# Optimization experiments

Measured on AMD Instinct MI355X. Metric: run time of the kernel, lower is better.

## Reference

```python
import jax, jax.numpy as jnp
import numpy as np

B, T, C = 4, 4096, 256
H = 4
D = C // H
EPS = 1e-5


def layer_norm(x, w, b):
    mean = x.mean(axis=-1, keepdims=True)
    var = x.var(axis=-1, keepdims=True)
    return w * (x - mean) / jnp.sqrt(var + EPS) + b


def setup_inputs() -> dict:
    key = jax.random.key(0)
    ks = jax.random.split(key, 8)
    s = lambda n: 1.0 / np.sqrt(n)
    return {
        "x": jax.random.normal(ks[0], (B, T, C), jnp.float32),
        "qkv_w": jax.random.normal(ks[1], (C, 3 * C), jnp.float32) * s(C),
        "qkv_b": jnp.zeros((3 * C,), jnp.float32),
        "proj_w": jax.random.normal(ks[2], (C, C), jnp.float32) * s(C),
        "proj_b": jnp.zeros((C,), jnp.float32),
        "n1_w": jnp.ones((C,), jnp.float32),
        "n1_b": jnp.zeros((C,), jnp.float32),
        "ffn_w1": jax.random.normal(ks[3], (C, 3 * C), jnp.float32) * s(C),
        "ffn_b1": jnp.zeros((3 * C,), jnp.float32),
        "ffn_w2": jax.random.normal(ks[4], (3 * C, C), jnp.float32) * s(3 * C),
        "ffn_b2": jnp.zeros((C,), jnp.float32),
        "n2_w": jnp.ones((C,), jnp.float32),
        "n2_b": jnp.zeros((C,), jnp.float32),
    }


def reference(x, qkv_w, qkv_b, proj_w, proj_b, n1_w, n1_b,
              ffn_w1, ffn_b1, ffn_w2, ffn_b2, n2_w, n2_b):
    scale = D ** -0.5
    qkv = (x @ qkv_w + qkv_b).reshape(B, T, 3, H, D)
    qkv = jnp.transpose(qkv, (2, 0, 3, 1, 4))  # [3, B, H, T, D]
    q, k, v = qkv[0], qkv[1], qkv[2]
    attn = jnp.einsum('bhtd,bhsd->bhts', q, k) * scale  # [B,H,T,T]
    attn = jax.nn.softmax(attn, axis=-1)
    out = jnp.einsum('bhts,bhsd->bhtd', attn, v)
    out = jnp.transpose(out, (0, 2, 1, 3)).reshape(B, T, C)
    attn_out = out @ proj_w + proj_b
    x = layer_norm(x + attn_out, n1_w, n1_b)
    h = jax.nn.gelu(x @ ffn_w1 + ffn_b1, approximate=False)
    ffn_out = h @ ffn_w2 + ffn_b2
    x = layer_norm(x + ffn_out, n2_w, n2_b)
    return x
```

## Files before the change

### kernel.cpp

```cpp
#include <hip/hip_runtime.h>
#include <cstdint>
#include <cstddef>

typedef __bf16 bf16;
typedef __bf16 bf16x8 __attribute__((ext_vector_type(8)));
typedef __bf16 bf16x4 __attribute__((ext_vector_type(4)));
typedef _Float16 f16;
typedef _Float16 f16x4 __attribute__((ext_vector_type(4)));
typedef _Float16 f16x8 __attribute__((ext_vector_type(8)));
typedef __fp16 fp16x2 __attribute__((ext_vector_type(2)));
typedef float f32x4 __attribute__((ext_vector_type(4)));

#define DEV static __device__ __forceinline__
#if __has_builtin(__builtin_amdgcn_exp2f)
#define EXP2(x) __builtin_amdgcn_exp2f(x)
#else
#define EXP2(x) exp2f(x)
#endif
#define QSCALE 0.18033688011112042f

DEV float gelu_exact(float v) {
  return 0.5f * v * (1.0f + erff(v * 0.70710678118654752f));
}

__global__ void cvt_w_kernel(const float* __restrict__ qkv_w, bf16* __restrict__ qwt,
                             const float* __restrict__ proj_w, bf16* __restrict__ pwt,
                             const float* __restrict__ f1w, bf16* __restrict__ f1wt,
                             const float* __restrict__ f2w, bf16* __restrict__ f2wt) {
  int blk = blockIdx.x;
  const float* w; bf16* o; int K, N;
  if (blk < 48)       { w = qkv_w;  o = qwt;  K = 256; N = 768; }
  else if (blk < 64)  { w = proj_w; o = pwt;  K = 256; N = 256; blk -= 48; }
  else if (blk < 112) { w = f1w;    o = f1wt; K = 256; N = 768; blk -= 64; }
  else                { w = f2w;    o = f2wt; K = 768; N = 256; blk -= 112; }
  const int ntiles = N >> 6;
  const int kt = blk / ntiles, nt = blk - kt * ntiles;
  const int k0 = kt * 64, n0 = nt * 64;
  __shared__ float tile[64][65];
  const int tid = threadIdx.x;
#pragma unroll
  for (int j = 0; j < 4; ++j) {
    const int c = j * 256 + tid;
    const int row = c >> 4, c4 = (c & 15) * 4;
    const float4 v = *(const float4*)(w + (size_t)(k0 + row) * N + n0 + c4);
    tile[row][c4] = v.x; tile[row][c4 + 1] = v.y;
    tile[row][c4 + 2] = v.z; tile[row][c4 + 3] = v.w;
  }
  __syncthreads();
#pragma unroll
  for (int j = 0; j < 4; ++j) {
    const int c = j * 256 + tid;
    const int n = c >> 4, k4 = (c & 15) * 4;
    bf16x4 ov;
#pragma unroll
    for (int i = 0; i < 4; ++i) ov[i] = (bf16)tile[k4 + i][n];
    *(bf16x4*)(o + (size_t)(n0 + n) * K + k0 + k4) = ov;
  }
}

__global__ __launch_bounds__(256, 2)
void gemm_qkv_kernel(const float* __restrict__ A, const bf16* __restrict__ Wt,
                     const float* __restrict__ bias, bf16* __restrict__ qb,
                     bf16* __restrict__ kb, f16* __restrict__ vt) {
  const int tid = threadIdx.x;
  const int wave = tid >> 6, lane = tid & 63;
  const int quad = lane >> 4, l15 = lane & 15;
  const int m0 = blockIdx.y * 128, n0 = blockIdx.x * 128;
  const int mw = (wave >> 1) * 64, nw = (wave & 1) * 64;
  const int K = 256;

  __shared__ bf16 lA[128 * 72];
  __shared__ bf16 lB[128 * 72];

  f32x4 acc[4][4] = {};

  for (int k0 = 0; k0 < K; k0 += 64) {
#pragma unroll
    for (int j = 0; j < 4; ++j) {
      const int c = j * 256 + tid;
      const int row = c >> 3, kc = (c & 7) * 8;
      const float* ax = A + (size_t)(m0 + row) * K + k0 + kc;
      const float4 a0 = *(const float4*)(ax);
      const float4 a1 = *(const float4*)(ax + 4);
      bf16x8 ab;
      ab[0] = (bf16)a0.x; ab[1] = (bf16)a0.y; ab[2] = (bf16)a0.z; ab[3] = (bf16)a0.w;
      ab[4] = (bf16)a1.x; ab[5] = (bf16)a1.y; ab[6] = (bf16)a1.z; ab[7] = (bf16)a1.w;
      *(bf16x8*)(lA + row * 72 + kc) = ab;
      *(uint4*)(lB + row * 72 + kc) =
          *(const uint4*)(Wt + (size_t)(n0 + row) * K + k0 + kc);
    }
    __syncthreads();
#pragma unroll
    for (int ks = 0; ks < 2; ++ks) {
      bf16x8 af[4], bfm[4];
#pragma unroll
      for (int i = 0; i < 4; ++i)
        af[i] = *(const bf16x8*)(lA + (mw + i * 16 + l15) * 72 + ks * 32 + quad * 8);
#pragma unroll
      for (int j = 0; j < 4; ++j)
        bfm[j] = *(const bf16x8*)(lB + (nw + j * 16 + l15) * 72 + ks * 32 + quad * 8);
#pragma unroll
      for (int i = 0; i < 4; ++i)
#pragma unroll
        for (int j = 0; j < 4; ++j)
          acc[i][j] = __builtin_amdgcn_mfma_f32_16x16x32_bf16(af[i], bfm[j],
                                                              acc[i][j], 0, 0, 0);
    }
    __syncthreads();
  }

  const bool isV = (n0 >= 512);
#pragma unroll
  for (int i = 0; i < 4; ++i) {
#pragma unroll
    for (int j = 0; j < 4; ++j) {
      const int n = n0 + nw + j * 16 + l15;
      const float bs = bias[n];
      if (isV) {
        const int m = m0 + mw + i * 16 + quad * 4;
        const int b = m >> 12, t = m & 4095;
        const int h = (n >> 6) & 3, d = n & 63;
        const int tp = (t & ~31) | (((t >> 2) & 3) << 3) | (((t >> 4) & 1) << 2);
        f16x4 hv;
#pragma unroll
        for (int r = 0; r < 4; ++r) hv[r] = (f16)(acc[i][j][r] + bs);
        *(f16x4*)(vt + (size_t)((b * 4 + h) * 64 + d) * 4096 + tp) = hv;
      } else {
        const int s = n >> 8, cc = n & 255, h = cc >> 6, d = cc & 63;
#pragma unroll
        for (int r = 0; r < 4; ++r) {
          const int m = m0 + mw + i * 16 + quad * 4 + r;
          const int b = m >> 12, t = m & 4095;
          const float v = acc[i][j][r] + bs;
          const size_t idx = (size_t)((b * 4 + h) * 4096 + t) * 64 + d;
          if (s == 0) qb[idx] = (bf16)(v * QSCALE);
          else        kb[idx] = (bf16)v;
        }
      }
    }
  }
}

__global__ __launch_bounds__(256, 2)
void attn_kernel(const bf16* __restrict__ q, const bf16* __restrict__ k,
                 const f16* __restrict__ vt, bf16* __restrict__ o) {
  const int tid = threadIdx.x;
  const int wave = tid >> 6, lane = tid & 63;
  const int quad = lane >> 4, l15 = lane & 15;
  const int bh = blockIdx.y;
  const int q0 = blockIdx.x * 128;
  __shared__ bf16 lK[2][64 * 72];
  __shared__ f16  lV[2][64 * 72];

  bf16x8 qa0[2], qa1[2];
#pragma unroll
  for (int s = 0; s < 2; ++s) {
    const bf16* qp =
        q + ((size_t)bh * 4096 + q0 + wave * 32 + s * 16 + l15) * 64 + quad * 8;
    qa0[s] = *(const bf16x8*)(qp);
    qa1[s] = *(const bf16x8*)(qp + 32);
  }

  const int row0 = tid >> 3, off = (tid & 7) * 8;
  const bf16* kp = k + ((size_t)bh * 4096 + row0) * 64 + off;
  const f16*  vp = vt + ((size_t)bh * 64 + row0) * 4096 + off;
  const int lidx = row0 * 72 + off;

  *(uint4*)(lK[0] + lidx)            = *(const uint4*)(kp);
  *(uint4*)(lK[0] + lidx + 32 * 72)  = *(const uint4*)(kp + 32 * 64);
  *(uint4*)(lV[0] + lidx)            = *(const uint4*)(vp);
  *(uint4*)(lV[0] + lidx + 32 * 72)  = *(const uint4*)(vp + 32 * 4096);

  f32x4 accO[2][4] = {};
  f32x4 accD[2] = {};
  const f16x8 vone8 = {(f16)1.0f, (f16)1.0f, (f16)1.0f, (f16)1.0f,
                       (f16)1.0f, (f16)1.0f, (f16)1.0f, (f16)1.0f};
  uint4 pk0, pk1, pv0, pv1;

  for (int it = 0; it < 64; ++it) {
    const int cur = it & 1;
    if (it + 1 < 64) {
      const bf16* kn = kp + (size_t)(it + 1) * 64 * 64;
      const f16*  vn = vp + (it + 1) * 64;
      pk0 = *(const uint4*)(kn);
      pk1 = *(const uint4*)(kn + 32 * 64);
      pv0 = *(const uint4*)(vn);
      pv1 = *(const uint4*)(vn + 32 * 4096);
    }
    __syncthreads();

    f32x4 sf[2][4];
#pragma unroll
    for (int c = 0; c < 4; ++c) {
      const bf16x8 kb0 = *(const bf16x8*)(lK[cur] + (c * 16 + l15) * 72 + quad * 8);
      const bf16x8 kb1 = *(const bf16x8*)(lK[cur] + (c * 16 + l15) * 72 + 32 + quad * 8);
#pragma unroll
      for (int s = 0; s < 2; ++s) {
        f32x4 t = {};
        t = __builtin_amdgcn_mfma_f32_16x16x32_bf16(kb0, qa0[s], t, 0, 0, 0);
        t = __builtin_amdgcn_mfma_f32_16x16x32_bf16(kb1, qa1[s], t, 0, 0, 0);
        sf[s][c] = t;
      }
    }

    f16x8 pa[2][2];
#pragma unroll
    for (int s = 0; s < 2; ++s)
#pragma unroll
      for (int c2 = 0; c2 < 2; ++c2) {
        union { fp16x2 h2[4]; f16x8 h8; } u;
        u.h2[0] = __builtin_amdgcn_cvt_pkrtz(EXP2(sf[s][2 * c2][0]),
                                             EXP2(sf[s][2 * c2][1]));
        u.h2[1] = __builtin_amdgcn_cvt_pkrtz(EXP2(sf[s][2 * c2][2]),
                                             EXP2(sf[s][2 * c2][3]));
        u.h2[2] = __builtin_amdgcn_cvt_pkrtz(EXP2(sf[s][2 * c2 + 1][0]),
                                             EXP2(sf[s][2 * c2 + 1][1]));
        u.h2[3] = __builtin_amdgcn_cvt_pkrtz(EXP2(sf[s][2 * c2 + 1][2]),
                                             EXP2(sf[s][2 * c2 + 1][3]));
        pa[s][c2] = u.h8;
      }

#pragma unroll
    for (int s = 0; s < 2; ++s)
#pragma unroll
      for (int c2 = 0; c2 < 2; ++c2)
        accD[s] = __builtin_amdgcn_mfma_f32_16x16x32_f16(pa[s][c2], vone8,
                                                         accD[s], 0, 0, 0);

#pragma unroll
    for (int c2 = 0; c2 < 2; ++c2) {
#pragma unroll
      for (int n = 0; n < 4; ++n) {
        const f16x8 vb =
            *(const f16x8*)(lV[cur] + (n * 16 + l15) * 72 + c2 * 32 + quad * 8);
#pragma unroll
        for (int s = 0; s < 2; ++s)
          accO[s][n] = __builtin_amdgcn_mfma_f32_16x16x32_f16(pa[s][c2], vb,
                                                              accO[s][n], 0, 0, 0);
      }
    }

    if (it + 1 < 64) {
      *(uint4*)(lK[cur ^ 1] + lidx)           = pk0;
      *(uint4*)(lK[cur ^ 1] + lidx + 32 * 72) = pk1;
      *(uint4*)(lV[cur ^ 1] + lidx)           = pv0;
      *(uint4*)(lV[cur ^ 1] + lidx + 32 * 72) = pv1;
    }
  }

  const int b = bh >> 2, h = bh & 3;
#pragma unroll
  for (int s = 0; s < 2; ++s) {
    float inv[4];
#pragma unroll
    for (int r = 0; r < 4; ++r) inv[r] = 1.0f / accD[s][r];
#pragma unroll
    for (int n = 0; n < 4; ++n)
#pragma unroll
      for (int r = 0; r < 4; ++r) {
        const int t = q0 + wave * 32 + s * 16 + quad * 4 + r;
        o[(size_t)(b * 4096 + t) * 256 + h * 64 + n * 16 + l15] =
            (bf16)(accO[s][n][r] * inv[r]);
      }
  }
}

__global__ __launch_bounds__(256, 2)
void gemm_ffn1_kernel(const bf16* __restrict__ A, const bf16* __restrict__ Wt,
                      const float* __restrict__ bias, bf16* __restrict__ ob) {
  const int tid = threadIdx.x;
  const int wave = tid >> 6, lane = tid & 63;
  const int quad = lane >> 4, l15 = lane & 15;
  const int m0 = blockIdx.y * 128, n0 = blockIdx.x * 128;
  const int mw = (wave >> 1) * 64, nw = (wave & 1) * 64;
  const int K = 256;

  __shared__ bf16 lA[128 * 72];
  __shared__ bf16 lB[128 * 72];

  f32x4 acc[4][4] = {};

  for (int k0 = 0; k0 < K; k0 += 64) {
#pragma unroll
    for (int j = 0; j < 4; ++j) {
      const int c = j * 256 + tid;
      const int row = c >> 3, kc = (c & 7) * 8;
      *(uint4*)(lA + row * 72 + kc) =
          *(const uint4*)(A + (size_t)(m0 + row) * K + k0 + kc);
      *(uint4*)(lB + row * 72 + kc) =
          *(const uint4*)(Wt + (size_t)(n0 + row) * K + k0 + kc);
    }
    __syncthreads();
#pragma unroll
    for (int ks = 0; ks < 2; ++ks) {
      bf16x8 af[4], bfm[4];
#pragma unroll
      for (int i = 0; i < 4; ++i)
        af[i] = *(const bf16x8*)(lA + (mw + i * 16 + l15) * 72 + ks * 32 + quad * 8);
#pragma unroll
      for (int j = 0; j < 4; ++j)
        bfm[j] = *(const bf16x8*)(lB + (nw + j * 16 + l15) * 72 + ks * 32 + quad * 8);
#pragma unroll
      for (int i = 0; i < 4; ++i)
#pragma unroll
        for (int j = 0; j < 4; ++j)
          acc[i][j] = __builtin_amdgcn_mfma_f32_16x16x32_bf16(af[i], bfm[j],
                                                              acc[i][j], 0, 0, 0);
    }
    __syncthreads();
  }

#pragma unroll
  for (int i = 0; i < 4; ++i) {
#pragma unroll
    for (int j = 0; j < 4; ++j) {
      const int n = n0 + nw + j * 16 + l15;
      const float bs = bias[n];
#pragma unroll
      for (int r = 0; r < 4; ++r) {
        const int m = m0 + mw + i * 16 + quad * 4 + r;
        ob[(size_t)m * 768 + n] = (bf16)gelu_exact(acc[i][j][r] + bs);
      }
    }
  }
}

template <int KTILES, bool RESID_BF16, bool WRITE_F, bool WRITE_B>
__global__ __launch_bounds__(256, 3)
void gemm_ln_kernel(const bf16* __restrict__ A, const bf16* __restrict__ Wt,
                    const float* __restrict__ bias, const void* __restrict__ Rv,
                    const float* __restrict__ lw, const float* __restrict__ lb,
                    float* __restrict__ outf, bf16* __restrict__ outb) {
  const int tid = threadIdx.x;
  const int wave = tid >> 6, lane = tid & 63;
  const int quad = lane >> 4, l15 = lane & 15;
  const int m0 = blockIdx.x * 32;
  const int nw = wave * 64;
  const int K = KTILES * 64;
  __shared__ bf16 lA[32 * 72];
  __shared__ bf16 lB[256 * 72];
  __shared__ float lnsum[4][32];
  __shared__ float lnsq[4][32];
  __shared__ float lnstat[32][2];
  f32x4 acc[2][4] = {};

  for (int kt = 0; kt < KTILES; ++kt) {
    const int k0 = kt * 64;
    {
      const int row = tid >> 3, kc = (tid & 7) * 8;
      *(uint4*)(lA + row * 72 + kc) =
          *(const uint4*)(A + (size_t)(m0 + row) * K + k0 + kc);
    }
#pragma unroll
    for (int j = 0; j < 8; ++j) {
      const int c = j * 256 + tid;
      const int row = c >> 3, kc = (c & 7) * 8;
      *(uint4*)(lB + row * 72 + kc) =
          *(const uint4*)(Wt + (size_t)row * K + k0 + kc);
    }
    __syncthreads();
#pragma unroll
    for (int ks = 0; ks < 2; ++ks) {
      bf16x8 af[2], bfm[4];
#pragma unroll
      for (int i = 0; i < 2; ++i)
        af[i] = *(const bf16x8*)(lA + (i * 16 + l15) * 72 + ks * 32 + quad * 8);
#pragma unroll
      for (int j = 0; j < 4; ++j)
        bfm[j] = *(const bf16x8*)(lB + (nw + j * 16 + l15) * 72 + ks * 32 + quad * 8);
#pragma unroll
      for (int i = 0; i < 2; ++i)
#pragma unroll
        for (int j = 0; j < 4; ++j)
          acc[i][j] = __builtin_amdgcn_mfma_f32_16x16x32_bf16(af[i], bfm[j],
                                                              acc[i][j], 0, 0, 0);
    }
    __syncthreads();
  }

  float bv[4], lwv[4], lbv[4];
#pragma unroll
  for (int j = 0; j < 4; ++j) {
    const int col = nw + 16 * j + l15;
    bv[j] = bias[col]; lwv[j] = lw[col]; lbv[j] = lb[col];
  }
#pragma unroll
  for (int i = 0; i < 2; ++i) {
    float ps[4] = {}, pq[4] = {};
#pragma unroll
    for (int j = 0; j < 4; ++j) {
#pragma unroll
      for (int r = 0; r < 4; ++r) {
        const int m = m0 + 16 * i + 4 * quad + r;
        const size_t ri = (size_t)m * 256 + nw + 16 * j + l15;
        const float rv = RESID_BF16 ? (float)((const bf16*)Rv)[ri]
                                    : ((const float*)Rv)[ri];
        const float v = acc[i][j][r] + bv[j] + rv;
        acc[i][j][r] = v;
        ps[r] += v;
        pq[r] += v * v;
      }
    }
#pragma unroll
    for (int r = 0; r < 4; ++r) {
#pragma unroll
      for (int mm = 1; mm < 16; mm <<= 1) {
        ps[r] += __shfl_xor(ps[r], mm, 64);
        pq[r] += __shfl_xor(pq[r], mm, 64);
      }
      if (l15 == 0) {
        lnsum[wave][16 * i + 4 * quad + r] = ps[r];
        lnsq[wave][16 * i + 4 * quad + r] = pq[r];
      }
    }
  }
  __syncthreads();
  if (tid < 32) {
    const float s = lnsum[0][tid] + lnsum[1][tid] + lnsum[2][tid] + lnsum[3][tid];
    const float sq = lnsq[0][tid] + lnsq[1][tid] + lnsq[2][tid] + lnsq[3][tid];
    const float mean = s * (1.0f / 256.0f);
    const float var = sq * (1.0f / 256.0f) - mean * mean;
    lnstat[tid][0] = mean;
    lnstat[tid][1] = rsqrtf(var + 1e-5f);
  }
  __syncthreads();
#pragma unroll
  for (int i = 0; i < 2; ++i) {
#pragma unroll
    for (int r = 0; r < 4; ++r) {
      const int row = 16 * i + 4 * quad + r;
      const float mean = lnstat[row][0], rstd = lnstat[row][1];
#pragma unroll
      for (int j = 0; j < 4; ++j) {
        const float ov = (acc[i][j][r] - mean) * rstd * lwv[j] + lbv[j];
        const size_t gi = (size_t)(m0 + row) * 256 + nw + 16 * j + l15;
        if constexpr (WRITE_F) outf[gi] = ov;
        if constexpr (WRITE_B) outb[gi] = (bf16)ov;
      }
    }
  }
}

extern "C" void kernel_launch(void* const* d_in, const int* in_sizes, int n_in,
                              void* d_out, int out_size, void* d_ws, size_t ws_size,
                              hipStream_t stream) {
  const float* x      = (const float*)d_in[0];
  const float* qkv_w  = (const float*)d_in[1];
  const float* qkv_b  = (const float*)d_in[2];
  const float* proj_w = (const float*)d_in[3];
  const float* proj_b = (const float*)d_in[4];
  const float* n1_w   = (const float*)d_in[5];
  const float* n1_b   = (const float*)d_in[6];
  const float* ffn_w1 = (const float*)d_in[7];
  const float* ffn_b1 = (const float*)d_in[8];
  const float* ffn_w2 = (const float*)d_in[9];
  const float* ffn_b2 = (const float*)d_in[10];
  const float* n2_w   = (const float*)d_in[11];
  const float* n2_b   = (const float*)d_in[12];
  float* out = (float*)d_out;

  char* ws = (char*)d_ws;
  bf16*  qwt  = (bf16*)(ws + 0);
  bf16*  pwt  = (bf16*)(ws + 393216);
  bf16*  f1wt = (bf16*)(ws + 524288);
  bf16*  f2wt = (bf16*)(ws + 917504);
  bf16*  qb   = (bf16*)(ws + 1310720);
  bf16*  kb   = (bf16*)(ws + 9699328);
  f16*   vtb  = (f16*)(ws + 18087936);
  bf16*  attn = (bf16*)(ws + 26476544);
  bf16*  x1b  = (bf16*)(ws + 34865152);
  bf16*  hbuf = (bf16*)(ws + 1310720);

  cvt_w_kernel<<<160, 256, 0, stream>>>(qkv_w, qwt, proj_w, pwt,
                                        ffn_w1, f1wt, ffn_w2, f2wt);
  gemm_qkv_kernel<<<dim3(6, 128), 256, 0, stream>>>(x, qwt, qkv_b, qb, kb, vtb);
  attn_kernel<<<dim3(32, 16), 256, 0, stream>>>(qb, kb, vtb, attn);
  gemm_ln_kernel<4, false, false, true><<<512, 256, 0, stream>>>(
      attn, pwt, proj_b, x, n1_w, n1_b, nullptr, x1b);
  gemm_ffn1_kernel<<<dim3(6, 128), 256, 0, stream>>>(x1b, f1wt, ffn_b1, hbuf);
  gemm_ln_kernel<12, true, true, false><<<512, 256, 0, stream>>>(
      hbuf, f2wt, ffn_b2, x1b, n2_w, n2_b, out, nullptr);
}
```

Measured before the change: 238.1 us.

## Pre-convert x to bf16 and give each attention wave 64 query rows

The input x is converted to bf16 once, in extra blocks of the weight-conversion kernel, so the QKV GEMM loads bf16 directly instead of converting fp32 inside every N-tile block. The attention kernel now runs 2 waves of 128 threads per block, each handling 64 query rows instead of 32. This doubles K/V reuse per LDS load and halves the number of waves sharing each tile, at the cost of more accumulator registers. Launch bounds for the two GEMMs are raised to 3 blocks per CU to increase occupancy.

```diff
diff --git a/kernel.cpp b/kernel.cpp
--- a/kernel.cpp
+++ b/kernel.cpp
@@ -26,8 +26,20 @@
 __global__ void cvt_w_kernel(const float* __restrict__ qkv_w, bf16* __restrict__ qwt,
                              const float* __restrict__ proj_w, bf16* __restrict__ pwt,
                              const float* __restrict__ f1w, bf16* __restrict__ f1wt,
-                             const float* __restrict__ f2w, bf16* __restrict__ f2wt) {
+                             const float* __restrict__ f2w, bf16* __restrict__ f2wt,
+                             const float* __restrict__ x, bf16* __restrict__ xb) {
   int blk = blockIdx.x;
+  const int tid = threadIdx.x;
+  if (blk >= 160) {
+    const size_t i = ((size_t)(blk - 160) * 256 + tid) * 8;
+    const float4 a0 = *(const float4*)(x + i);
+    const float4 a1 = *(const float4*)(x + i + 4);
+    bf16x8 v;
+    v[0] = (bf16)a0.x; v[1] = (bf16)a0.y; v[2] = (bf16)a0.z; v[3] = (bf16)a0.w;
+    v[4] = (bf16)a1.x; v[5] = (bf16)a1.y; v[6] = (bf16)a1.z; v[7] = (bf16)a1.w;
+    *(bf16x8*)(xb + i) = v;
+    return;
+  }
   const float* w; bf16* o; int K, N;
   if (blk < 48)       { w = qkv_w;  o = qwt;  K = 256; N = 768; }
   else if (blk < 64)  { w = proj_w; o = pwt;  K = 256; N = 256; blk -= 48; }
@@ -37,7 +49,6 @@
   const int kt = blk / ntiles, nt = blk - kt * ntiles;
   const int k0 = kt * 64, n0 = nt * 64;
   __shared__ float tile[64][65];
-  const int tid = threadIdx.x;
 #pragma unroll
   for (int j = 0; j < 4; ++j) {
     const int c = j * 256 + tid;
@@ -58,8 +69,8 @@
   }
 }
 
-__global__ __launch_bounds__(256, 2)
-void gemm_qkv_kernel(const float* __restrict__ A, const bf16* __restrict__ Wt,
+__global__ __launch_bounds__(256, 3)
+void gemm_qkv_kernel(const bf16* __restrict__ A, const bf16* __restrict__ Wt,
                      const float* __restrict__ bias, bf16* __restrict__ qb,
                      bf16* __restrict__ kb, f16* __restrict__ vt) {
   const int tid = threadIdx.x;
@@ -79,13 +90,8 @@
     for (int j = 0; j < 4; ++j) {
       const int c = j * 256 + tid;
       const int row = c >> 3, kc = (c & 7) * 8;
-      const float* ax = A + (size_t)(m0 + row) * K + k0 + kc;
-      const float4 a0 = *(const float4*)(ax);
-      const float4 a1 = *(const float4*)(ax + 4);
-      bf16x8 ab;
-      ab[0] = (bf16)a0.x; ab[1] = (bf16)a0.y; ab[2] = (bf16)a0.z; ab[3] = (bf16)a0.w;
-      ab[4] = (bf16)a1.x; ab[5] = (bf16)a1.y; ab[6] = (bf16)a1.z; ab[7] = (bf16)a1.w;
-      *(bf16x8*)(lA + row * 72 + kc) = ab;
+      *(uint4*)(lA + row * 72 + kc) =
+          *(const uint4*)(A + (size_t)(m0 + row) * K + k0 + kc);
       *(uint4*)(lB + row * 72 + kc) =
           *(const uint4*)(Wt + (size_t)(n0 + row) * K + k0 + kc);
     }
@@ -141,7 +147,7 @@
   }
 }
 
-__global__ __launch_bounds__(256, 2)
+__global__ __launch_bounds__(128, 2)
 void attn_kernel(const bf16* __restrict__ q, const bf16* __restrict__ k,
                  const f16* __restrict__ vt, bf16* __restrict__ o) {
   const int tid = threadIdx.x;
@@ -152,105 +158,100 @@
   __shared__ bf16 lK[2][64 * 72];
   __shared__ f16  lV[2][64 * 72];
 
-  bf16x8 qa0[2], qa1[2];
-#pragma unroll
-  for (int s = 0; s < 2; ++s) {
+  bf16x8 qa0[4], qa1[4];
+#pragma unroll
+  for (int s = 0; s < 4; ++s) {
     const bf16* qp =
-        q + ((size_t)bh * 4096 + q0 + wave * 32 + s * 16 + l15) * 64 + quad * 8;
+        q + ((size_t)bh * 4096 + q0 + wave * 64 + s * 16 + l15) * 64 + quad * 8;
     qa0[s] = *(const bf16x8*)(qp);
     qa1[s] = *(const bf16x8*)(qp + 32);
   }
 
-  const int row0 = tid >> 3, off = (tid & 7) * 8;
-  const bf16* kp = k + ((size_t)bh * 4096 + row0) * 64 + off;
-  const f16*  vp = vt + ((size_t)bh * 64 + row0) * 4096 + off;
-  const int lidx = row0 * 72 + off;
-
-  *(uint4*)(lK[0] + lidx)            = *(const uint4*)(kp);
-  *(uint4*)(lK[0] + lidx + 32 * 72)  = *(const uint4*)(kp + 32 * 64);
-  *(uint4*)(lV[0] + lidx)            = *(const uint4*)(vp);
-  *(uint4*)(lV[0] + lidx + 32 * 72)  = *(const uint4*)(vp + 32 * 4096);
-
-  f32x4 accO[2][4] = {};
-  f32x4 accD[2] = {};
+  const int r0 = tid >> 3, off = (tid & 7) * 8;
+  const bf16* kp = k + ((size_t)bh * 4096 + r0) * 64 + off;
+  const f16*  vp = vt + ((size_t)bh * 64 + r0) * 4096 + off;
+  const int lidx = r0 * 72 + off;
+
+#pragma unroll
+  for (int j = 0; j < 4; ++j) {
+    *(uint4*)(lK[0] + lidx + j * 16 * 72) = *(const uint4*)(kp + j * 16 * 64);
+    *(uint4*)(lV[0] + lidx + j * 16 * 72) = *(const uint4*)(vp + j * 16 * 4096);
+  }
+
+  f32x4 accO[4][4] = {};
+  f32x4 accD[4] = {};
   const f16x8 vone8 = {(f16)1.0f, (f16)1.0f, (f16)1.0f, (f16)1.0f,
                        (f16)1.0f, (f16)1.0f, (f16)1.0f, (f16)1.0f};
-  uint4 pk0, pk1, pv0, pv1;
+  uint4 pk[4], pv[4];
 
   for (int it = 0; it < 64; ++it) {
     const int cur = it & 1;
     if (it + 1 < 64) {
-      const bf16* kn = kp + (size_t)(it + 1) * 64 * 64;
+      const bf16* kn = kp + (size_t)(it + 1) * 4096;
       const f16*  vn = vp + (it + 1) * 64;
-      pk0 = *(const uint4*)(kn);
-      pk1 = *(const uint4*)(kn + 32 * 64);
-      pv0 = *(const uint4*)(vn);
-      pv1 = *(const uint4*)(vn + 32 * 4096);
-    }
-    __syncthreads();
-
-    f32x4 sf[2][4];
-#pragma unroll
-    for (int c = 0; c < 4; ++c) {
-      const bf16x8 kb0 = *(const bf16x8*)(lK[cur] + (c * 16 + l15) * 72 + quad * 8);
-      const bf16x8 kb1 = *(const bf16x8*)(lK[cur] + (c * 16 + l15) * 72 + 32 + quad * 8);
-#pragma unroll
-      for (int s = 0; s < 2; ++s) {
-        f32x4 t = {};
-        t = __builtin_amdgcn_mfma_f32_16x16x32_bf16(kb0, qa0[s], t, 0, 0, 0);
-        t = __builtin_amdgcn_mfma_f32_16x16x32_bf16(kb1, qa1[s], t, 0, 0, 0);
-        sf[s][c] = t;
-      }
-    }
-
-    f16x8 pa[2][2];
-#pragma unroll
-    for (int s = 0; s < 2; ++s)
-#pragma unroll
-      for (int c2 = 0; c2 < 2; ++c2) {
+#pragma unroll
+      for (int j = 0; j < 4; ++j) {
+        pk[j] = *(const uint4*)(kn + j * 1024);
+        pv[j] = *(const uint4*)(vn + j * 16 * 4096);
+      }
+    }
+    __syncthreads();
+
+#pragma unroll
+    for (int c2 = 0; c2 < 2; ++c2) {
+      f32x4 sf[4][2];
+#pragma unroll
+      for (int cc = 0; cc < 2; ++cc) {
+        const int c = c2 * 2 + cc;
+        const bf16x8 kb0 =
+            *(const bf16x8*)(lK[cur] + (c * 16 + l15) * 72 + quad * 8);
+        const bf16x8 kb1 =
+            *(const bf16x8*)(lK[cur] + (c * 16 + l15) * 72 + 32 + quad * 8);
+#pragma unroll
+        for (int s = 0; s < 4; ++s) {
+          f32x4 t = {};
+          t = __builtin_amdgcn_mfma_f32_16x16x32_bf16(kb0, qa0[s], t, 0, 0, 0);
+          t = __builtin_amdgcn_mfma_f32_16x16x32_bf16(kb1, qa1[s], t, 0, 0, 0);
+          sf[s][cc] = t;
+        }
+      }
+      f16x8 pa[4];
+#pragma unroll
+      for (int s = 0; s < 4; ++s) {
         union { fp16x2 h2[4]; f16x8 h8; } u;
-        u.h2[0] = __builtin_amdgcn_cvt_pkrtz(EXP2(sf[s][2 * c2][0]),
-                                             EXP2(sf[s][2 * c2][1]));
-        u.h2[1] = __builtin_amdgcn_cvt_pkrtz(EXP2(sf[s][2 * c2][2]),
-                                             EXP2(sf[s][2 * c2][3]));
-        u.h2[2] = __builtin_amdgcn_cvt_pkrtz(EXP2(sf[s][2 * c2 + 1][0]),
-                                             EXP2(sf[s][2 * c2 + 1][1]));
-        u.h2[3] = __builtin_amdgcn_cvt_pkrtz(EXP2(sf[s][2 * c2 + 1][2]),
-                                             EXP2(sf[s][2 * c2 + 1][3]));
-        pa[s][c2] = u.h8;
-      }
-
-#pragma unroll
-    for (int s = 0; s < 2; ++s)
-#pragma unroll
-      for (int c2 = 0; c2 < 2; ++c2)
-        accD[s] = __builtin_amdgcn_mfma_f32_16x16x32_f16(pa[s][c2], vone8,
+        u.h2[0] = __builtin_amdgcn_cvt_pkrtz(EXP2(sf[s][0][0]), EXP2(sf[s][0][1]));
+        u.h2[1] = __builtin_amdgcn_cvt_pkrtz(EXP2(sf[s][0][2]), EXP2(sf[s][0][3]));
+        u.h2[2] = __builtin_amdgcn_cvt_pkrtz(EXP2(sf[s][1][0]), EXP2(sf[s][1][1]));
+        u.h2[3] = __builtin_amdgcn_cvt_pkrtz(EXP2(sf[s][1][2]), EXP2(sf[s][1][3]));
+        pa[s] = u.h8;
+      }
+#pragma unroll
+      for (int s = 0; s < 4; ++s)
+        accD[s] = __builtin_amdgcn_mfma_f32_16x16x32_f16(pa[s], vone8,
                                                          accD[s], 0, 0, 0);
-
-#pragma unroll
-    for (int c2 = 0; c2 < 2; ++c2) {
 #pragma unroll
       for (int n = 0; n < 4; ++n) {
         const f16x8 vb =
             *(const f16x8*)(lV[cur] + (n * 16 + l15) * 72 + c2 * 32 + quad * 8);
 #pragma unroll
-        for (int s = 0; s < 2; ++s)
-          accO[s][n] = __builtin_amdgcn_mfma_f32_16x16x32_f16(pa[s][c2], vb,
+        for (int s = 0; s < 4; ++s)
+          accO[s][n] = __builtin_amdgcn_mfma_f32_16x16x32_f16(pa[s], vb,
                                                               accO[s][n], 0, 0, 0);
       }
     }
 
     if (it + 1 < 64) {
-      *(uint4*)(lK[cur ^ 1] + lidx)           = pk0;
-      *(uint4*)(lK[cur ^ 1] + lidx + 32 * 72) = pk1;
-      *(uint4*)(lV[cur ^ 1] + lidx)           = pv0;
-      *(uint4*)(lV[cur ^ 1] + lidx + 32 * 72) = pv1;
+#pragma unroll
+      for (int j = 0; j < 4; ++j) {
+        *(uint4*)(lK[cur ^ 1] + lidx + j * 16 * 72) = pk[j];
+        *(uint4*)(lV[cur ^ 1] + lidx + j * 16 * 72) = pv[j];
+      }
     }
   }
 
   const int b = bh >> 2, h = bh & 3;
 #pragma unroll
-  for (int s = 0; s < 2; ++s) {
+  for (int s = 0; s < 4; ++s) {
     float inv[4];
 #pragma unroll
     for (int r = 0; r < 4; ++r) inv[r] = 1.0f / accD[s][r];
@@ -258,14 +259,14 @@
     for (int n = 0; n < 4; ++n)
 #pragma unroll
       for (int r = 0; r < 4; ++r) {
-        const int t = q0 + wave * 32 + s * 16 + quad * 4 + r;
+        const int t = q0 + wave * 64 + s * 16 + quad * 4 + r;
         o[(size_t)(b * 4096 + t) * 256 + h * 64 + n * 16 + l15] =
             (bf16)(accO[s][n][r] * inv[r]);
       }
   }
 }
 
-__global__ __launch_bounds__(256, 2)
+__global__ __launch_bounds__(256, 3)
 void gemm_ffn1_kernel(const bf16* __restrict__ A, const bf16* __restrict__ Wt,
                       const float* __restrict__ bias, bf16* __restrict__ ob) {
   const int tid = threadIdx.x;
@@ -470,11 +471,12 @@
   bf16*  attn = (bf16*)(ws + 26476544);
   bf16*  x1b  = (bf16*)(ws + 34865152);
   bf16*  hbuf = (bf16*)(ws + 1310720);
-
-  cvt_w_kernel<<<160, 256, 0, stream>>>(qkv_w, qwt, proj_w, pwt,
-                                        ffn_w1, f1wt, ffn_w2, f2wt);
-  gemm_qkv_kernel<<<dim3(6, 128), 256, 0, stream>>>(x, qwt, qkv_b, qb, kb, vtb);
-  attn_kernel<<<dim3(32, 16), 256, 0, stream>>>(qb, kb, vtb, attn);
+  bf16*  xb   = (bf16*)(ws + 34865152);
+
+  cvt_w_kernel<<<2208, 256, 0, stream>>>(qkv_w, qwt, proj_w, pwt,
+                                         ffn_w1, f1wt, ffn_w2, f2wt, x, xb);
+  gemm_qkv_kernel<<<dim3(6, 128), 256, 0, stream>>>(xb, qwt, qkv_b, qb, kb, vtb);
+  attn_kernel<<<dim3(32, 16), 128, 0, stream>>>(qb, kb, vtb, attn);
   gemm_ln_kernel<4, false, false, true><<<512, 256, 0, stream>>>(
       attn, pwt, proj_b, x, n1_w, n1_b, nullptr, x1b);
   gemm_ffn1_kernel<<<dim3(6, 128), 256, 0, stream>>>(x1b, f1wt, ffn_b1, hbuf);
```

Result: slower. 312.8 us (+31.4%).
